# Kernel optimization log

Measured on AMD Instinct MI355X. Metric: run time of the kernel, lower is better.

The kernel has to match this reference:

```python
import jax, jax.numpy as jnp
import numpy as np

B, M, C, S, SD, K, H = 32, 448, 384, 512, 128, 8, 8
DH = C // H
EPS = 1e-5
NEG_SLOPE = 0.2


def setup_inputs() -> dict:
    key = jax.random.key(0)
    ks = iter(jax.random.split(key, 32))
    nrm = lambda shape, scale=0.05: (jax.random.normal(next(ks), shape, jnp.float32) * scale)
    inp = {
        'q': jax.random.normal(next(ks), (B, M, C), jnp.float32),
        'coarse': jax.random.normal(next(ks), (B, M, 3), jnp.float32),
        'skeleton': jax.random.normal(next(ks), (B, S, 3), jnp.float32),
        # GraphConv 1: 3 -> 64 (root weight, rel/neighbor weight, bias)
        'gc1_wroot': nrm((3, 64), 0.3), 'gc1_wrel': nrm((3, 64), 0.3), 'gc1_b': jnp.zeros((64,), jnp.float32),
        # GraphConv 2: 64 -> SD
        'gc2_wroot': nrm((64, SD), 0.1), 'gc2_wrel': nrm((64, SD), 0.1), 'gc2_b': jnp.zeros((SD,), jnp.float32),
        # skeleton_projection: SD -> C
        'proj_w': nrm((SD, C), 0.08), 'proj_b': jnp.zeros((C,), jnp.float32),
        # MultiheadAttention (torch layout: in_proj (3C, C), out_proj (C, C))
        'attn_in_w': nrm((3 * C, C), 0.05), 'attn_in_b': jnp.zeros((3 * C,), jnp.float32),
        'attn_out_w': nrm((C, C), 0.05), 'attn_out_b': jnp.zeros((C,), jnp.float32),
        # increase_dim: Conv1d(C,1024,1) + BN(1024) + LeakyReLU + Conv1d(1024,1024,1)
        'inc1_w': nrm((1024, C), 0.05), 'inc1_b': jnp.zeros((1024,), jnp.float32),
        'bn_g': jnp.ones((1024,), jnp.float32), 'bn_b': jnp.zeros((1024,), jnp.float32),
        'bn_m': jnp.zeros((1024,), jnp.float32), 'bn_v': jnp.ones((1024,), jnp.float32),
        'inc2_w': nrm((1024, 1024), 0.03), 'inc2_b': jnp.zeros((1024,), jnp.float32),
        # reduce_map: Linear(C + 1024 + 3, C)
        'red_w': nrm((1024 + C + 3, C), 0.03), 'red_b': jnp.zeros((C,), jnp.float32),
    }
    return inp


def _knn_idx(pts):
    # pts: [B,S,3]; per-batch kNN (self excluded), matching knn_graph(k=K, batch=...)
    d2 = jnp.sum((pts[:, :, None, :] - pts[:, None, :, :]) ** 2, axis=-1)  # [B,S,S]
    d2 = d2 + jnp.eye(S, dtype=pts.dtype)[None] * 1e10                       # mask self
    _, idx = jax.lax.top_k(-d2, K)                                           # [B,S,K]
    return idx


def _graph_conv(x, idx, wroot, wrel, b):
    # GraphConv (PyG, aggr='add'): out_i = x_i Wroot + (sum_{j in N(i)} x_j) Wrel + b
    nb = jax.vmap(lambda f, i: f[i])(x, idx)   # [B,S,K,F]
    agg = nb.sum(axis=2)                       # [B,S,F]
    return x @ wroot + agg @ wrel + b


def reference(q, coarse, skeleton, gc1_wroot, gc1_wrel, gc1_b, gc2_wroot, gc2_wrel, gc2_b,
              proj_w, proj_b, attn_in_w, attn_in_b, attn_out_w, attn_out_b,
              inc1_w, inc1_b, bn_g, bn_b, bn_m, bn_v, inc2_w, inc2_b, red_w, red_b):
    # --- skeleton branch: knn graph + 2-layer GraphConv + max-pool + projection ---
    idx = _knn_idx(skeleton)
    h = _graph_conv(skeleton, idx, gc1_wroot, gc1_wrel, gc1_b)
    h = jax.nn.relu(h)
    h = _graph_conv(h, idx, gc2_wroot, gc2_wrel, gc2_b)        # [B,S,SD]
    proxy = jnp.max(h, axis=1)                                  # [B,SD]
    proxy = proxy @ proj_w + proj_b                             # [B,C]
    kv = jnp.broadcast_to(proxy[:, None, :], (B, M, C))         # expanded proxies

    # --- cross attention (torch nn.MultiheadAttention math) ---
    wq, wk, wv = attn_in_w[:C], attn_in_w[C:2 * C], attn_in_w[2 * C:]
    bq, bk, bv = attn_in_b[:C], attn_in_b[C:2 * C], attn_in_b[2 * C:]
    qh = (q @ wq.T + bq).reshape(B, M, H, DH)
    kh = (kv @ wk.T + bk).reshape(B, M, H, DH)
    vh = (kv @ wv.T + bv).reshape(B, M, H, DH)
    scores = jnp.einsum('bmhd,bnhd->bhmn', qh, kh) / jnp.sqrt(jnp.float32(DH))
    attn = jax.nn.softmax(scores, axis=-1)
    ctx = jnp.einsum('bhmn,bnhd->bmhd', attn, vh).reshape(B, M, C)
    q = ctx @ attn_out_w.T + attn_out_b                         # fused features [B,M,C]

    # --- increase_dim (1x1 conv == matmul) + BN(eval) + LeakyReLU + 1x1 conv ---
    g = jnp.einsum('bmc,oc->bmo', q, inc1_w) + inc1_b           # [B,M,1024]
    g = bn_g * (g - bn_m) * jax.lax.rsqrt(bn_v + EPS) + bn_b
    g = jnp.where(g >= 0, g, NEG_SLOPE * g)
    g = jnp.einsum('bmc,oc->bmo', g, inc2_w) + inc2_b
    global_feature = jnp.max(g, axis=1)                         # [B,1024]

    # --- concat + reduce_map ---
    rebuild = jnp.concatenate([jnp.broadcast_to(global_feature[:, None, :], (B, M, 1024)), q, coarse], axis=-1)
    out = rebuild @ red_w + red_b                               # [B,M,C]
    return out
```

## Files before the change

kernel.cpp:

```cpp
#include <hip/hip_runtime.h>

#define NB 32
#define MM 448
#define CC 384
#define SS 512
#define KNN 8

#define WS_IDX   0u
#define WS_H1    524288u
#define WS_PMAX  (WS_H1 + 4194304u)
#define WS_Q     (WS_PMAX + 262144u)
#define WS_Y     (WS_Q + 49152u)
#define WS_G2    (WS_Y + 131072u)
#define WS_BASEP (WS_G2 + 131072u)

__global__ __launch_bounds__(256) void k_knn_gc1(
    const float* __restrict__ skel,
    const float* __restrict__ w1root, const float* __restrict__ w1rel,
    const float* __restrict__ b1,
    int* __restrict__ idx_ws, float* __restrict__ h1_ws)
{
  int b   = blockIdx.x >> 7;
  int grp = blockIdx.x & 127;
  __shared__ __align__(16) float4 sk[SS];
  const float* sb = skel + b * SS * 3;
  for (int t = threadIdx.x; t < SS; t += 256)
    sk[t] = make_float4(sb[t*3+0], sb[t*3+1], sb[t*3+2], 0.f);
  __syncthreads();

  int wave = threadIdx.x >> 6, lane = threadIdx.x & 63;
  int i = grp * 4 + wave;
  float4 pi = sk[i];

  float bd[KNN];
#pragma unroll
  for (int t = 0; t < KNN; t++) {
    int j = lane + (t << 6);
    float4 p = sk[j];
    float d2;
    {
#pragma clang fp contract(off)
      float dx = pi.x - p.x, dy = pi.y - p.y, dz = pi.z - p.z;
      d2 = (dx*dx + dy*dy) + dz*dz;
    }
    bd[t] = (j == i) ? 3e38f : d2;
  }

  int win[KNN];
  int* idx_base = idx_ws + (size_t)(b*SS + i) * KNN;
#pragma unroll
  for (int t = 0; t < KNN; t++) {
    float bestd = bd[0]; int bests = 0;
#pragma unroll
    for (int s = 1; s < KNN; s++)
      if (bd[s] < bestd) { bestd = bd[s]; bests = s; }
    int bestj = lane + (bests << 6);
#pragma unroll
    for (int m = 1; m < 64; m <<= 1) {
      float od = __shfl_xor(bestd, m, 64);
      int   oj = __shfl_xor(bestj, m, 64);
      if (od < bestd || (od == bestd && oj < bestj)) { bestd = od; bestj = oj; }
    }
    win[t] = bestj;
    if (lane == t) idx_base[t] = bestj;
    if ((bestj & 63) == lane) {
      int sl = bestj >> 6;
#pragma unroll
      for (int s = 0; s < KNN; s++) if (s == sl) bd[s] = 3e38f;
    }
  }

  float a0 = 0.f, a1 = 0.f, a2 = 0.f;
#pragma unroll
  for (int t = 0; t < KNN; t++) {
    float4 n = sk[win[t]];
    a0 += n.x; a1 += n.y; a2 += n.z;
  }

  int c = lane;
  float h = b1[c] + pi.x*w1root[c] + pi.y*w1root[64+c] + pi.z*w1root[128+c]
                  + a0*w1rel[c]   + a1*w1rel[64+c]   + a2*w1rel[128+c];
  h = fmaxf(h, 0.f);
  h1_ws[(size_t)(b*SS + i) * 64 + lane] = h;
}

__global__ __launch_bounds__(256) void k_gc2_max(
    const float* __restrict__ h1_ws, const int* __restrict__ idx_ws,
    const float* __restrict__ w2root, const float* __restrict__ w2rel,
    const float* __restrict__ b2, float* __restrict__ pmax)
{
  int b = blockIdx.x >> 4, chunk = blockIdx.x & 15;
  int r0 = chunk * 32;
  __shared__ __align__(16) float X[32*129];
  __shared__ __align__(16) float Wt[32*128];
  __shared__ float mred[8*128];
  __shared__ int nbs[32*KNN];

  const float* h1b = h1_ws + (size_t)b * SS * 64;
  nbs[threadIdx.x] = idx_ws[(b*SS + r0)*KNN + threadIdx.x];
#pragma unroll
  for (int p = 0; p < 8; p++) {
    int idx = threadIdx.x + 256*p;
    int r = idx >> 6, k = idx & 63;
    X[r*129 + k] = h1b[(r0 + r)*64 + k];
  }
  __syncthreads();
#pragma unroll
  for (int p = 0; p < 8; p++) {
    int idx = threadIdx.x + 256*p;
    int r = idx >> 6, k = idx & 63;
    const int* nb = nbs + r*KNN;
    float s = 0.f;
#pragma unroll
    for (int j = 0; j < KNN; j++) s += h1b[nb[j]*64 + k];
    X[r*129 + 64 + k] = s;
  }

  int rg = threadIdx.x >> 5, cg = threadIdx.x & 31;
  float acc[4][4];
#pragma unroll
  for (int r = 0; r < 4; r++)
#pragma unroll
    for (int u = 0; u < 4; u++) acc[r][u] = 0.f;

  const float* wsrc[4] = { w2root, w2root + 32*128, w2rel, w2rel + 32*128 };
#pragma unroll 1
  for (int ch = 0; ch < 4; ch++) {
    __syncthreads();
    const float* ws = wsrc[ch];
#pragma unroll
    for (int p = 0; p < 16; p++) {
      int idx = threadIdx.x + 256*p;
      Wt[idx] = ws[idx];
    }
    __syncthreads();
    int kb = ch * 32;
    const float* xr0 = X + (rg*4+0)*129 + kb;
    const float* xr1 = X + (rg*4+1)*129 + kb;
    const float* xr2 = X + (rg*4+2)*129 + kb;
    const float* xr3 = X + (rg*4+3)*129 + kb;
#pragma unroll 4
    for (int k = 0; k < 32; k++) {
      float4 w4 = *(const float4*)(Wt + k*128 + cg*4);
      float x0 = xr0[k], x1 = xr1[k], x2 = xr2[k], x3 = xr3[k];
      acc[0][0] += x0*w4.x; acc[0][1] += x0*w4.y; acc[0][2] += x0*w4.z; acc[0][3] += x0*w4.w;
      acc[1][0] += x1*w4.x; acc[1][1] += x1*w4.y; acc[1][2] += x1*w4.z; acc[1][3] += x1*w4.w;
      acc[2][0] += x2*w4.x; acc[2][1] += x2*w4.y; acc[2][2] += x2*w4.z; acc[2][3] += x2*w4.w;
      acc[3][0] += x3*w4.x; acc[3][1] += x3*w4.y; acc[3][2] += x3*w4.z; acc[3][3] += x3*w4.w;
    }
  }
#pragma unroll
  for (int u = 0; u < 4; u++)
    mred[rg*128 + cg*4 + u] =
      fmaxf(fmaxf(acc[0][u], acc[1][u]), fmaxf(acc[2][u], acc[3][u]));
  __syncthreads();
  if (threadIdx.x < 128) {
    int col = threadIdx.x;
    float mx = mred[col];
#pragma unroll
    for (int g = 1; g < 8; g++) mx = fmaxf(mx, mred[g*128 + col]);
    pmax[(size_t)(b*16 + chunk)*128 + col] = mx + b2[col];
  }
}

__global__ __launch_bounds__(256) void k_mid(
    const float* __restrict__ pmax,
    const float* __restrict__ proj_w, const float* __restrict__ proj_b,
    const float* __restrict__ aiw, const float* __restrict__ aib,
    const float* __restrict__ aow, const float* __restrict__ aob,
    const float* __restrict__ i1w, const float* __restrict__ i1b,
    const float* __restrict__ bng, const float* __restrict__ bnb,
    const float* __restrict__ bnm, const float* __restrict__ bnv,
    float* __restrict__ q_ws, float* __restrict__ y_ws)
{
  int b = blockIdx.x >> 2, sl = blockIdx.x & 3;
  int t = threadIdx.x;
  __shared__ __align__(16) float proxy[128];
  __shared__ __align__(16) float kv[CC];
  __shared__ __align__(16) float vv[CC];
  __shared__ __align__(16) float qv[CC];

  if (t < 128) {
    float m = -3e38f;
    for (int ch = 0; ch < 16; ch++)
      m = fmaxf(m, pmax[(size_t)(b*16 + ch)*128 + t]);
    proxy[t] = m;
  }
  __syncthreads();
  for (int c = t; c < CC; c += 256) {
    float acc = proj_b[c];
    for (int s = 0; s < 128; s++) acc += proxy[s] * proj_w[s*CC + c];
    kv[c] = acc;
  }
  __syncthreads();
  for (int o = t; o < CC; o += 256) {
    const float* wr = aiw + (size_t)(2*CC + o) * CC;
    float acc = aib[2*CC + o];
#pragma unroll 8
    for (int k = 0; k < CC; k += 4) {
      float4 w4 = *(const float4*)(wr + k);
      float4 x4 = *(const float4*)(kv + k);
      acc += w4.x*x4.x + w4.y*x4.y + w4.z*x4.z + w4.w*x4.w;
    }
    vv[o] = acc;
  }
  __syncthreads();
  for (int o = t; o < CC; o += 256) {
    const float* wr = aow + (size_t)o * CC;
    float acc = aob[o];
#pragma unroll 8
    for (int k = 0; k < CC; k += 4) {
      float4 w4 = *(const float4*)(wr + k);
      float4 x4 = *(const float4*)(vv + k);
      acc += w4.x*x4.x + w4.y*x4.y + w4.z*x4.z + w4.w*x4.w;
    }
    qv[o] = acc;
    if (sl == 0) q_ws[b*CC + o] = acc;
  }
  __syncthreads();
  {
    int o = sl*256 + t;
    const float* wr = i1w + (size_t)o * CC;
    float acc = i1b[o];
#pragma unroll 8
    for (int k = 0; k < CC; k += 4) {
      float4 w4 = *(const float4*)(wr + k);
      float4 x4 = *(const float4*)(qv + k);
      acc += w4.x*x4.x + w4.y*x4.y + w4.z*x4.z + w4.w*x4.w;
    }
    float z = bng[o] * (acc - bnm[o]) * rsqrtf(bnv[o] + 1e-5f) + bnb[o];
    y_ws[b*1024 + o] = (z >= 0.f) ? z : 0.2f * z;
  }
}

__global__ __launch_bounds__(256) void k_inc2(
    const float* __restrict__ y_ws, const float* __restrict__ inc2_w,
    const float* __restrict__ inc2_b, float* __restrict__ g2_ws)
{
  int b = blockIdx.x >> 4, og = blockIdx.x & 15;
  int t = threadIdx.x;
  int o = og*64 + (t >> 2), qq = t & 3;
  __shared__ __align__(16) float xs[1024];
  for (int i = t; i < 1024; i += 256) xs[i] = y_ws[b*1024 + i];
  __syncthreads();
  const float* wr = inc2_w + (size_t)o * 1024 + qq*256;
  const float* xr = xs + qq*256;
  float acc = 0.f;
#pragma unroll 8
  for (int kk = 0; kk < 256; kk += 4) {
    float4 w4 = *(const float4*)(wr + kk);
    float4 x4 = *(const float4*)(xr + kk);
    acc += w4.x*x4.x + w4.y*x4.y + w4.z*x4.z + w4.w*x4.w;
  }
  acc += __shfl_xor(acc, 1, 64);
  acc += __shfl_xor(acc, 2, 64);
  if (qq == 0) g2_ws[b*1024 + o] = acc + inc2_b[o];
}

__global__ __launch_bounds__(256) void k_base(
    const float* __restrict__ g2_ws, const float* __restrict__ q_ws,
    const float* __restrict__ red_w, float* __restrict__ basep)
{
  int b = blockIdx.x >> 3;
  int o0 = (blockIdx.x & 7) * 64;
  b = blockIdx.x;
  o0 = blockIdx.y * 64;
  int wv = threadIdx.x >> 6, lane = threadIdx.x & 63;
  __shared__ __align__(16) float X[1408];
  __shared__ float part[4][64];
  for (int i = threadIdx.x; i < 1408; i += 256)
    X[i] = (i < 1024) ? g2_ws[b*1024 + i] : q_ws[b*CC + (i - 1024)];
  __syncthreads();
  int k0 = wv * 352;
  float acc = 0.f;
  const float* wbase = red_w + o0 + lane;
#pragma unroll 4
  for (int k = 0; k < 352; k++)
    acc += X[k0 + k] * wbase[(size_t)(k0 + k) * CC];
  part[wv][lane] = acc;
  __syncthreads();
  if (threadIdx.x < 64) {
    float s = part[0][lane] + part[1][lane] + part[2][lane] + part[3][lane];
    basep[b*CC + o0 + lane] = s;
  }
}

__global__ __launch_bounds__(256) void k_out(
    const float* __restrict__ basep, const float* __restrict__ red_b,
    const float* __restrict__ red_w, const float* __restrict__ coarse,
    float* __restrict__ out)
{
  int gid = blockIdx.x * 256 + threadIdx.x;
  int c4 = gid % 96;
  int row = gid / 96;
  int b = row / 448;
  int c = c4 * 4;
  float4 p0 = *(const float4*)(basep + b*CC + c);
  float4 rb = *(const float4*)(red_b + c);
  const float* cr = coarse + (size_t)row * 3;
  float cx = cr[0], cy = cr[1], cz = cr[2];
  float4 w0 = *(const float4*)(red_w + (size_t)1408*CC + c);
  float4 w1 = *(const float4*)(red_w + (size_t)1409*CC + c);
  float4 w2 = *(const float4*)(red_w + (size_t)1410*CC + c);
  float4 o4;
  o4.x = p0.x + rb.x + cx*w0.x + cy*w1.x + cz*w2.x;
  o4.y = p0.y + rb.y + cx*w0.y + cy*w1.y + cz*w2.y;
  o4.z = p0.z + rb.z + cx*w0.z + cy*w1.z + cz*w2.z;
  o4.w = p0.w + rb.w + cx*w0.w + cy*w1.w + cz*w2.w;
  *(float4*)(out + (size_t)row*CC + c) = o4;
}

extern "C" void kernel_launch(void* const* d_in, const int* in_sizes, int n_in,
                              void* d_out, int out_size, void* d_ws, size_t ws_size,
                              hipStream_t stream)
{
  (void)in_sizes; (void)n_in; (void)out_size; (void)ws_size;
  const float* coarse = (const float*)d_in[1];
  const float* skel   = (const float*)d_in[2];
  const float* g1wr   = (const float*)d_in[3];
  const float* g1wl   = (const float*)d_in[4];
  const float* g1b    = (const float*)d_in[5];
  const float* g2wr   = (const float*)d_in[6];
  const float* g2wl   = (const float*)d_in[7];
  const float* g2b    = (const float*)d_in[8];
  const float* projw  = (const float*)d_in[9];
  const float* projb  = (const float*)d_in[10];
  const float* aiw    = (const float*)d_in[11];
  const float* aib    = (const float*)d_in[12];
  const float* aow    = (const float*)d_in[13];
  const float* aob    = (const float*)d_in[14];
  const float* i1w    = (const float*)d_in[15];
  const float* i1b    = (const float*)d_in[16];
  const float* bng    = (const float*)d_in[17];
  const float* bnb    = (const float*)d_in[18];
  const float* bnm    = (const float*)d_in[19];
  const float* bnv    = (const float*)d_in[20];
  const float* i2w    = (const float*)d_in[21];
  const float* i2b    = (const float*)d_in[22];
  const float* redw   = (const float*)d_in[23];
  const float* redb   = (const float*)d_in[24];
  float* out = (float*)d_out;

  char* ws = (char*)d_ws;
  int*   idx_ws = (int*)(ws + WS_IDX);
  float* h1_ws  = (float*)(ws + WS_H1);
  float* pmax   = (float*)(ws + WS_PMAX);
  float* q_ws   = (float*)(ws + WS_Q);
  float* y_ws   = (float*)(ws + WS_Y);
  float* g2_ws  = (float*)(ws + WS_G2);
  float* basep  = (float*)(ws + WS_BASEP);

  k_knn_gc1<<<4096, 256, 0, stream>>>(skel, g1wr, g1wl, g1b, idx_ws, h1_ws);
  k_gc2_max<<<512, 256, 0, stream>>>(h1_ws, idx_ws, g2wr, g2wl, g2b, pmax);
  k_mid<<<128, 256, 0, stream>>>(pmax, projw, projb, aiw, aib, aow, aob,
                                 i1w, i1b, bng, bnb, bnm, bnv, q_ws, y_ws);
  k_inc2<<<512, 256, 0, stream>>>(y_ws, i2w, i2b, g2_ws);
  k_base<<<dim3(32, 6), 256, 0, stream>>>(g2_ws, q_ws, redw, basep);
  k_out<<<5376, 256, 0, stream>>>(basep, redb, redw, coarse, out);
}
```

Measured before the change: 284.2 us.

## Split mid chain into two wider kernels and fuse base with output write

Splits the serial k_mid kernel (128 blocks) into k_chainA, which computes the V projection over 384 blocks using 8-way split-K with shuffle reductions, and k_chainB, which computes out_proj and inc1/BN/LeakyReLU over 256 blocks with split-K dot products. This is meant to remove the long per-block serial GEMV latency. It also fuses the reduce_map base computation with the output broadcast kernel, dropping the basep round trip and one launch. The cost is redundant proxy/kv computation in every chainA block and an extra launch, and the fused output write now runs on only 192 blocks.

```diff
diff --git a/kernel.cpp b/kernel.cpp
--- a/kernel.cpp
+++ b/kernel.cpp
@@ -12,7 +12,7 @@
 #define WS_Q     (WS_PMAX + 262144u)
 #define WS_Y     (WS_Q + 49152u)
 #define WS_G2    (WS_Y + 131072u)
-#define WS_BASEP (WS_G2 + 131072u)
+#define WS_VV    WS_IDX
 
 __global__ __launch_bounds__(256) void k_knn_gc1(
     const float* __restrict__ skel,
@@ -163,73 +163,100 @@
   }
 }
 
-__global__ __launch_bounds__(256) void k_mid(
+__global__ __launch_bounds__(256) void k_chainA(
     const float* __restrict__ pmax,
-    const float* __restrict__ proj_w, const float* __restrict__ proj_b,
+    const float* __restrict__ projw, const float* __restrict__ projb,
     const float* __restrict__ aiw, const float* __restrict__ aib,
+    float* __restrict__ vv_ws)
+{
+  int b = blockIdx.x / 12, sl = blockIdx.x % 12;
+  int t = threadIdx.x;
+  __shared__ __align__(16) float proxy[128];
+  __shared__ __align__(16) float kv[CC];
+  if (t < 128) {
+    float m = -3e38f;
+    for (int ch = 0; ch < 16; ch++)
+      m = fmaxf(m, pmax[(size_t)(b*16 + ch)*128 + t]);
+    proxy[t] = m;
+  }
+  __syncthreads();
+  for (int c = t; c < CC; c += 256) {
+    float acc = projb[c];
+    for (int s = 0; s < 128; s++) acc += proxy[s] * projw[s*CC + c];
+    kv[c] = acc;
+  }
+  __syncthreads();
+  int o = sl*32 + (t >> 3), qq = t & 7;
+  const float* wr = aiw + (size_t)(2*CC + o) * CC + qq*48;
+  const float* xr = kv + qq*48;
+  float acc = 0.f;
+#pragma unroll
+  for (int k = 0; k < 48; k += 4) {
+    float4 w4 = *(const float4*)(wr + k);
+    float4 x4 = *(const float4*)(xr + k);
+    acc += w4.x*x4.x + w4.y*x4.y + w4.z*x4.z + w4.w*x4.w;
+  }
+  acc += __shfl_xor(acc, 1, 64);
+  acc += __shfl_xor(acc, 2, 64);
+  acc += __shfl_xor(acc, 4, 64);
+  if (qq == 0) vv_ws[b*CC + o] = acc + aib[2*CC + o];
+}
+
+__global__ __launch_bounds__(256) void k_chainB(
+    const float* __restrict__ vv_ws,
     const float* __restrict__ aow, const float* __restrict__ aob,
     const float* __restrict__ i1w, const float* __restrict__ i1b,
     const float* __restrict__ bng, const float* __restrict__ bnb,
     const float* __restrict__ bnm, const float* __restrict__ bnv,
     float* __restrict__ q_ws, float* __restrict__ y_ws)
 {
-  int b = blockIdx.x >> 2, sl = blockIdx.x & 3;
+  int b = blockIdx.x >> 3, sl = blockIdx.x & 7;
   int t = threadIdx.x;
-  __shared__ __align__(16) float proxy[128];
-  __shared__ __align__(16) float kv[CC];
   __shared__ __align__(16) float vv[CC];
   __shared__ __align__(16) float qv[CC];
-
-  if (t < 128) {
-    float m = -3e38f;
-    for (int ch = 0; ch < 16; ch++)
-      m = fmaxf(m, pmax[(size_t)(b*16 + ch)*128 + t]);
-    proxy[t] = m;
-  }
-  __syncthreads();
-  for (int c = t; c < CC; c += 256) {
-    float acc = proj_b[c];
-    for (int s = 0; s < 128; s++) acc += proxy[s] * proj_w[s*CC + c];
-    kv[c] = acc;
-  }
-  __syncthreads();
-  for (int o = t; o < CC; o += 256) {
-    const float* wr = aiw + (size_t)(2*CC + o) * CC;
-    float acc = aib[2*CC + o];
-#pragma unroll 8
-    for (int k = 0; k < CC; k += 4) {
+  for (int i = t; i < CC; i += 256) vv[i] = vv_ws[b*CC + i];
+  __syncthreads();
+  {
+    int qq = t & 3;
+    const float* xr = vv + qq*96;
+#pragma unroll 1
+    for (int r = 0; r < 6; r++) {
+      int o = r*64 + (t >> 2);
+      const float* wr = aow + (size_t)o * CC + qq*96;
+      float acc = 0.f;
+#pragma unroll
+      for (int k = 0; k < 96; k += 4) {
+        float4 w4 = *(const float4*)(wr + k);
+        float4 x4 = *(const float4*)(xr + k);
+        acc += w4.x*x4.x + w4.y*x4.y + w4.z*x4.z + w4.w*x4.w;
+      }
+      acc += __shfl_xor(acc, 1, 64);
+      acc += __shfl_xor(acc, 2, 64);
+      if (qq == 0) {
+        float v = acc + aob[o];
+        qv[o] = v;
+        if (sl == 0) q_ws[b*CC + o] = v;
+      }
+    }
+  }
+  __syncthreads();
+  {
+    int o = sl*128 + (t >> 1), qq = t & 1;
+    const float* wr = i1w + (size_t)o * CC + qq*192;
+    const float* xr = qv + qq*192;
+    float acc = 0.f;
+#pragma unroll 12
+    for (int k = 0; k < 192; k += 4) {
       float4 w4 = *(const float4*)(wr + k);
-      float4 x4 = *(const float4*)(kv + k);
+      float4 x4 = *(const float4*)(xr + k);
       acc += w4.x*x4.x + w4.y*x4.y + w4.z*x4.z + w4.w*x4.w;
     }
-    vv[o] = acc;
-  }
-  __syncthreads();
-  for (int o = t; o < CC; o += 256) {
-    const float* wr = aow + (size_t)o * CC;
-    float acc = aob[o];
-#pragma unroll 8
-    for (int k = 0; k < CC; k += 4) {
-      float4 w4 = *(const float4*)(wr + k);
-      float4 x4 = *(const float4*)(vv + k);
-      acc += w4.x*x4.x + w4.y*x4.y + w4.z*x4.z + w4.w*x4.w;
-    }
-    qv[o] = acc;
-    if (sl == 0) q_ws[b*CC + o] = acc;
-  }
-  __syncthreads();
-  {
-    int o = sl*256 + t;
-    const float* wr = i1w + (size_t)o * CC;
-    float acc = i1b[o];
-#pragma unroll 8
-    for (int k = 0; k < CC; k += 4) {
-      float4 w4 = *(const float4*)(wr + k);
-      float4 x4 = *(const float4*)(qv + k);
-      acc += w4.x*x4.x + w4.y*x4.y + w4.z*x4.z + w4.w*x4.w;
-    }
-    float z = bng[o] * (acc - bnm[o]) * rsqrtf(bnv[o] + 1e-5f) + bnb[o];
-    y_ws[b*1024 + o] = (z >= 0.f) ? z : 0.2f * z;
+    acc += __shfl_xor(acc, 1, 64);
+    if (qq == 0) {
+      float a = acc + i1b[o];
+      float z = bng[o] * (a - bnm[o]) * rsqrtf(bnv[o] + 1e-5f) + bnb[o];
+      y_ws[b*1024 + o] = (z >= 0.f) ? z : 0.2f * z;
+    }
   }
 }
 
@@ -257,17 +284,17 @@
   if (qq == 0) g2_ws[b*1024 + o] = acc + inc2_b[o];
 }
 
-__global__ __launch_bounds__(256) void k_base(
+__global__ __launch_bounds__(256) void k_base_out(
     const float* __restrict__ g2_ws, const float* __restrict__ q_ws,
-    const float* __restrict__ red_w, float* __restrict__ basep)
-{
-  int b = blockIdx.x >> 3;
-  int o0 = (blockIdx.x & 7) * 64;
-  b = blockIdx.x;
-  o0 = blockIdx.y * 64;
+    const float* __restrict__ red_w, const float* __restrict__ red_b,
+    const float* __restrict__ coarse, float* __restrict__ out)
+{
+  int b = blockIdx.x;
+  int o0 = blockIdx.y * 64;
   int wv = threadIdx.x >> 6, lane = threadIdx.x & 63;
   __shared__ __align__(16) float X[1408];
   __shared__ float part[4][64];
+  __shared__ __align__(16) float baseS[64];
   for (int i = threadIdx.x; i < 1408; i += 256)
     X[i] = (i < 1024) ? g2_ws[b*1024 + i] : q_ws[b*CC + (i - 1024)];
   __syncthreads();
@@ -279,35 +306,28 @@
     acc += X[k0 + k] * wbase[(size_t)(k0 + k) * CC];
   part[wv][lane] = acc;
   __syncthreads();
-  if (threadIdx.x < 64) {
-    float s = part[0][lane] + part[1][lane] + part[2][lane] + part[3][lane];
-    basep[b*CC + o0 + lane] = s;
-  }
-}
-
-__global__ __launch_bounds__(256) void k_out(
-    const float* __restrict__ basep, const float* __restrict__ red_b,
-    const float* __restrict__ red_w, const float* __restrict__ coarse,
-    float* __restrict__ out)
-{
-  int gid = blockIdx.x * 256 + threadIdx.x;
-  int c4 = gid % 96;
-  int row = gid / 96;
-  int b = row / 448;
-  int c = c4 * 4;
-  float4 p0 = *(const float4*)(basep + b*CC + c);
-  float4 rb = *(const float4*)(red_b + c);
-  const float* cr = coarse + (size_t)row * 3;
-  float cx = cr[0], cy = cr[1], cz = cr[2];
+  if (threadIdx.x < 64)
+    baseS[lane] = part[0][lane] + part[1][lane] + part[2][lane] + part[3][lane]
+                + red_b[o0 + lane];
+  __syncthreads();
+  int c4 = threadIdx.x & 15;
+  int r0 = threadIdx.x >> 4;
+  int c = o0 + c4*4;
+  float4 base4 = *(const float4*)(baseS + c4*4);
   float4 w0 = *(const float4*)(red_w + (size_t)1408*CC + c);
   float4 w1 = *(const float4*)(red_w + (size_t)1409*CC + c);
   float4 w2 = *(const float4*)(red_w + (size_t)1410*CC + c);
-  float4 o4;
-  o4.x = p0.x + rb.x + cx*w0.x + cy*w1.x + cz*w2.x;
-  o4.y = p0.y + rb.y + cx*w0.y + cy*w1.y + cz*w2.y;
-  o4.z = p0.z + rb.z + cx*w0.z + cy*w1.z + cz*w2.z;
-  o4.w = p0.w + rb.w + cx*w0.w + cy*w1.w + cz*w2.w;
-  *(float4*)(out + (size_t)row*CC + c) = o4;
+#pragma unroll 4
+  for (int m = r0; m < MM; m += 16) {
+    const float* cr = coarse + (size_t)(b*MM + m) * 3;
+    float cx = cr[0], cy = cr[1], cz = cr[2];
+    float4 o4;
+    o4.x = base4.x + cx*w0.x + cy*w1.x + cz*w2.x;
+    o4.y = base4.y + cx*w0.y + cy*w1.y + cz*w2.y;
+    o4.z = base4.z + cx*w0.z + cy*w1.z + cz*w2.z;
+    o4.w = base4.w + cx*w0.w + cy*w1.w + cz*w2.w;
+    *(float4*)(out + (size_t)(b*MM + m)*CC + c) = o4;
+  }
 }
 
 extern "C" void kernel_launch(void* const* d_in, const int* in_sizes, int n_in,
@@ -348,13 +368,13 @@
   float* q_ws   = (float*)(ws + WS_Q);
   float* y_ws   = (float*)(ws + WS_Y);
   float* g2_ws  = (float*)(ws + WS_G2);
-  float* basep  = (float*)(ws + WS_BASEP);
+  float* vv_ws  = (float*)(ws + WS_VV);
 
   k_knn_gc1<<<4096, 256, 0, stream>>>(skel, g1wr, g1wl, g1b, idx_ws, h1_ws);
   k_gc2_max<<<512, 256, 0, stream>>>(h1_ws, idx_ws, g2wr, g2wl, g2b, pmax);
-  k_mid<<<128, 256, 0, stream>>>(pmax, projw, projb, aiw, aib, aow, aob,
-                                 i1w, i1b, bng, bnb, bnm, bnv, q_ws, y_ws);
+  k_chainA<<<384, 256, 0, stream>>>(pmax, projw, projb, aiw, aib, vv_ws);
+  k_chainB<<<256, 256, 0, stream>>>(vv_ws, aow, aob, i1w, i1b,
+                                    bng, bnb, bnm, bnv, q_ws, y_ws);
   k_inc2<<<512, 256, 0, stream>>>(y_ws, i2w, i2b, g2_ws);
-  k_base<<<dim3(32, 6), 256, 0, stream>>>(g2_ws, q_ws, redw, basep);
-  k_out<<<5376, 256, 0, stream>>>(basep, redb, redw, coarse, out);
-}
+  k_base_out<<<dim3(32, 6), 256, 0, stream>>>(g2_ws, q_ws, redw, redb, coarse, out);
+}
```

Measured after the change: 267.7 us. 1.06x faster.
